# Kernel optimization log

Measured on AMD Instinct MI355X. Metric: run time of the kernel, lower is better.

The kernel has to match this reference:

```python
import jax, jax.numpy as jnp
import numpy as np

IN_FEA = 128
OUT_FEA = 128
ALPHA = 0.2  # LeakyReLU negative slope
NEG_INF = -1.0e12


def setup_inputs() -> dict:
    key = jax.random.key(0)
    k1, k2, k3, k4 = jax.random.split(key, 4)
    b, n = 8, 2048
    inp = jax.random.normal(k1, (b, n, IN_FEA), dtype=jnp.float32)
    adj = jax.random.randint(k2, (b, n, n), 0, 2, dtype=jnp.int32)
    # xavier_uniform with gain=1.414
    def xavier(k, shape, gain=1.414):
        fan_in, fan_out = shape[0], shape[1]
        limit = gain * np.sqrt(6.0 / (fan_in + fan_out))
        return jax.random.uniform(k, shape, jnp.float32, -limit, limit)
    W = xavier(k3, (IN_FEA, OUT_FEA))
    a = xavier(k4, (2 * OUT_FEA, 1))
    return {"inp": inp, "adj": adj, "W": W, "a": a}


def reference(inp, adj, W, a):
    # h: [b, n, d]
    h = jnp.matmul(inp, W)
    # Original builds [b, n*n, 2d] via repeat/view; equivalently split a into
    # a1 (applied to h_j, the 'chunks' half) and a2 (applied to h_i).
    d = h.shape[-1]
    a1 = a[:d, 0]   # [d]
    a2 = a[d:, 0]   # [d]
    f1 = jnp.einsum('bnd,d->bn', h, a1)  # contributes per-column (j)
    f2 = jnp.einsum('bnd,d->bn', h, a2)  # contributes per-row (i)
    e = jax.nn.leaky_relu(f2[:, :, None] + f1[:, None, :], negative_slope=ALPHA)  # [b, n, n]
    logits = jnp.where(adj > 0, e, NEG_INF)
    attention = jax.nn.softmax(logits, axis=-1)
    out_h = jnp.matmul(attention, h)
    out_h = jax.nn.elu(out_h) + h  # concat=True branch
    return out_h
```

## Files before the change

### kernel.cpp

```cpp
#include <hip/hip_runtime.h>
#include <hip/hip_bf16.h>

typedef __bf16 bf16x8 __attribute__((ext_vector_type(8)));
typedef float  f32x4  __attribute__((ext_vector_type(4)));

#define LRELU_ALPHA 0.2f
#define LOG2E 1.44269504088896340736f

__device__ __forceinline__ float fexp2(float x) {
#if __has_builtin(__builtin_amdgcn_exp2f)
    return __builtin_amdgcn_exp2f(x);
#else
    float r; asm("v_exp_f32 %0, %1" : "=v"(r) : "v"(x)); return r;
#endif
}

__device__ __forceinline__ void wg_barrier() {
    asm volatile("s_waitcnt lgkmcnt(0)" ::: "memory");
    __builtin_amdgcn_s_barrier();
    asm volatile("" ::: "memory");
}

__global__ __launch_bounds__(128) void gat_prep(
    const float* __restrict__ inp, const float* __restrict__ W,
    const float* __restrict__ a,
    __bf16* __restrict__ hb, float* __restrict__ f1, float* __restrict__ f2)
{
    const int r0 = blockIdx.x << 3;
    const int d  = threadIdx.x;
    __shared__ float sIn[8][128];
    __shared__ float sRed[8][4];
    #pragma unroll
    for (int r = 0; r < 8; ++r)
        sIn[r][d] = inp[(size_t)(r0 + r) * 128 + d];
    __syncthreads();

    float acc[8] = {0.f,0.f,0.f,0.f,0.f,0.f,0.f,0.f};
    #pragma unroll 4
    for (int k = 0; k < 128; ++k) {
        float wv = W[k * 128 + d];
        #pragma unroll
        for (int r = 0; r < 8; ++r) acc[r] += sIn[r][k] * wv;
    }

    const float a1 = a[d], a2 = a[128 + d];
    const int wv = d >> 6;
    #pragma unroll
    for (int r = 0; r < 8; ++r) {
        hb[(size_t)(r0 + r) * 128 + d] = (__bf16)acc[r];
        float t1 = acc[r] * a1;
        float t2 = acc[r] * a2;
        #pragma unroll
        for (int m = 1; m < 64; m <<= 1) {
            t1 += __shfl_xor(t1, m);
            t2 += __shfl_xor(t2, m);
        }
        if ((d & 63) == 0) { sRed[r][wv] = t1; sRed[r][2 + wv] = t2; }
    }
    __syncthreads();
    if (d < 8) {
        f1[r0 + d] = (sRed[d][0] + sRed[d][1]) * LOG2E;
        f2[r0 + d] = (sRed[d][2] + sRed[d][3]) * LOG2E;
    }
}

__global__ __launch_bounds__(256) void gat_f1max(
    const float* __restrict__ f1, float* __restrict__ f1max)
{
    const int b = blockIdx.x;
    const int t = threadIdx.x;
    float m = -1e30f;
    for (int j = t; j < 2048; j += 256) m = fmaxf(m, f1[b * 2048 + j]);
    #pragma unroll
    for (int k = 1; k < 64; k <<= 1) m = fmaxf(m, __shfl_xor(m, k));
    __shared__ float sm[4];
    if ((t & 63) == 0) sm[t >> 6] = m;
    __syncthreads();
    if (t == 0) f1max[b] = fmaxf(fmaxf(sm[0], sm[1]), fmaxf(sm[2], sm[3]));
}

__global__ __launch_bounds__(256) void gat_pack(
    const __bf16* __restrict__ hb, __bf16* __restrict__ pack)
{
    __shared__ __bf16 tile[64][72];
    const int tid = threadIdx.x;
    const int bidx = blockIdx.x;
    const int b  = bidx >> 6;
    const int tI = bidx & 63;
    const int n0 = (tI >> 1) << 6;
    const int d0 = (tI & 1) << 6;
    #pragma unroll
    for (int pass = 0; pass < 2; ++pass) {
        int row = (tid >> 3) + (pass << 5);
        int c   = (tid & 7) << 3;
        *(bf16x8*)&tile[row][c] =
            *(const bf16x8*)(hb + (size_t)(b * 2048 + n0 + row) * 128 + d0 + c);
    }
    __syncthreads();
    const int lane = tid & 63;
    const int il = lane & 15;
    const int kg = lane >> 4;
    #pragma unroll
    for (int pass = 0; pass < 2; ++pass) {
        const int f  = (tid >> 6) + (pass << 2);
        const int Dl = f >> 1;
        const int jh = f & 1;
        union { __bf16 e[8]; bf16x8 v; } u;
        #pragma unroll
        for (int e = 0; e < 8; ++e)
            u.e[e] = tile[(jh << 5) + (kg << 3) + e][(Dl << 4) + il];
        const size_t off = (((size_t)(b << 5) + (n0 >> 6)) << 13)
                         + ((size_t)((((d0 >> 4) + Dl) << 1) | jh) << 9)
                         + (lane << 3);
        *(bf16x8*)(pack + off) = u.v;
    }
}

__global__ __launch_bounds__(512, 4) void gat_attn13(
    const int* __restrict__ adj, const __bf16* __restrict__ pack,
    const float* __restrict__ f1g, const float* __restrict__ f2g,
    const float* __restrict__ f1maxg,
    float* __restrict__ out, __bf16* __restrict__ pO, float* __restrict__ pD)
{
    const int bid = ((blockIdx.x & 7) << 6) | (blockIdx.x >> 3);
    const int b  = bid >> 6;
    const int rg = (bid >> 2) & 15;
    const int jq = bid & 3;
    const int i0 = rg << 7;
    const int jb = jq << 9;
    const int tid = threadIdx.x;

    __shared__ float us[512];
    __shared__ float vs[512];
    __shared__ alignas(16) __bf16 Bs[2][4096];

    const int w    = tid >> 6;
    const int lane = tid & 63;
    const int il   = lane & 15;
    const int kg   = lane >> 4;

    if (tid < 128) {
        float4 fv = *(const float4*)&f1g[(b << 11) + jb + (tid << 2)];
        float4 uu, vv;
        uu.x = fexp2(fv.x); uu.y = fexp2(fv.y);
        uu.z = fexp2(fv.z); uu.w = fexp2(fv.w);
        vv.x = fexp2(LRELU_ALPHA * fv.x); vv.y = fexp2(LRELU_ALPHA * fv.y);
        vv.z = fexp2(LRELU_ALPHA * fv.z); vv.w = fexp2(LRELU_ALPHA * fv.w);
        *(float4*)&us[tid << 2] = uu;
        *(float4*)&vs[tid << 2] = vv;
    }

    const int row  = i0 + (w << 4) + il;
    const float fm  = f1maxg[b];
    const float f2v = f2g[(b << 11) + row];
    const float zM  = f2v + fm;
    const float M   = fmaxf(zM, LRELU_ALPHA * zM);
    const float ai_ = fexp2(f2v - M);
    const float bi_ = fexp2(__builtin_fmaf(LRELU_ALPHA, f2v, -M));

    const int* ap = adj + (((size_t)(b << 11) + row) << 11) + jb + (kg << 3);

    const __bf16* pkB = pack + (((size_t)(b << 5) + (jq << 3)) << 13)
                      + ((w << 1) << 9) + (lane << 3);

    f32x4 acc[8];
    #pragma unroll
    for (int D = 0; D < 8; ++D) acc[D] = (f32x4){0.f, 0.f, 0.f, 0.f};
    f32x4 accd = {0.f, 0.f, 0.f, 0.f};
    union { __bf16 e[8]; bf16x8 v; } ones;
    #pragma unroll
    for (int x = 0; x < 8; ++x) ones.e[x] = (__bf16)1.0f;
    const bf16x8 onesv = ones.v;

    int4 adjx[2], adjy[2];
    int4 sg = *(const int4*)(pkB);
    adjx[0] = *(const int4*)(ap);
    adjy[0] = *(const int4*)(ap + 4);
    adjx[1] = *(const int4*)(ap + 32);
    adjy[1] = *(const int4*)(ap + 36);
    *(int4*)&Bs[0][(w << 9) + (lane << 3)] = sg;
    sg = *(const int4*)(pkB + 512);

    wg_barrier();

    #pragma unroll
    for (int t = 0; t < 16; ++t) {
        const int cb = t & 1;

        bf16x8 Bf[8];
        #pragma unroll
        for (int D = 0; D < 8; ++D)
            Bf[D] = *(const bf16x8*)&Bs[cb][(D << 9) + (lane << 3)];

        const int4 ax = adjx[t & 1];
        const int4 ay = adjy[t & 1];
        const float4 u0 = *(const float4*)&us[t * 32 + (kg << 3)];
        const float4 u1 = *(const float4*)&us[t * 32 + (kg << 3) + 4];
        const float4 v0 = *(const float4*)&vs[t * 32 + (kg << 3)];
        const float4 v1 = *(const float4*)&vs[t * 32 + (kg << 3) + 4];
        union { __bf16 e[8]; bf16x8 v; } pa;
        pa.e[0] = (ax.x > 0) ? (__bf16)fmaxf(ai_ * u0.x, bi_ * v0.x) : (__bf16)0.f;
        pa.e[1] = (ax.y > 0) ? (__bf16)fmaxf(ai_ * u0.y, bi_ * v0.y) : (__bf16)0.f;
        pa.e[2] = (ax.z > 0) ? (__bf16)fmaxf(ai_ * u0.z, bi_ * v0.z) : (__bf16)0.f;
        pa.e[3] = (ax.w > 0) ? (__bf16)fmaxf(ai_ * u0.w, bi_ * v0.w) : (__bf16)0.f;
        pa.e[4] = (ay.x > 0) ? (__bf16)fmaxf(ai_ * u1.x, bi_ * v1.x) : (__bf16)0.f;
        pa.e[5] = (ay.y > 0) ? (__bf16)fmaxf(ai_ * u1.y, bi_ * v1.y) : (__bf16)0.f;
        pa.e[6] = (ay.z > 0) ? (__bf16)fmaxf(ai_ * u1.z, bi_ * v1.z) : (__bf16)0.f;
        pa.e[7] = (ay.w > 0) ? (__bf16)fmaxf(ai_ * u1.w, bi_ * v1.w) : (__bf16)0.f;

        if (t + 2 < 16) {
            adjx[t & 1] = *(const int4*)(ap + (t + 2) * 32);
            adjy[t & 1] = *(const int4*)(ap + (t + 2) * 32 + 4);
        }

        #pragma unroll
        for (int D = 0; D < 8; ++D)
            acc[D] = __builtin_amdgcn_mfma_f32_16x16x32_bf16(pa.v, Bf[D], acc[D], 0, 0, 0);
        accd = __builtin_amdgcn_mfma_f32_16x16x32_bf16(pa.v, onesv, accd, 0, 0, 0);

        if (t < 15) {
            *(int4*)&Bs[cb ^ 1][(w << 9) + (lane << 3)] = sg;
            if (t < 14)
                sg = *(const int4*)(pkB + (((t + 2) >> 1) << 13) + (((t + 2) & 1) << 9));
            wg_barrier();
        }
    }

    const int rowg = (b << 11) + i0 + (w << 4) + (kg << 2);
    if (jq == 0) {
        #pragma unroll
        for (int r = 0; r < 4; ++r) {
            const size_t base = (((size_t)rowg + r) << 7) + il;
            #pragma unroll
            for (int D = 0; D < 8; ++D)
                out[base + (D << 4)] = acc[D][r];
        }
    } else {
        __bf16* po = pO + ((size_t)(jq - 1) << 21);
        #pragma unroll
        for (int r = 0; r < 4; ++r) {
            const size_t base = (((size_t)rowg + r) << 7) + il;
            #pragma unroll
            for (int D = 0; D < 8; ++D)
                po[base + (D << 4)] = (__bf16)acc[D][r];
        }
    }
    if (il == 0) {
        #pragma unroll
        for (int r = 0; r < 4; ++r)
            pD[(jq << 14) + rowg + r] = accd[r];
    }
}

__global__ __launch_bounds__(256) void gat_combine(
    float* io, const __bf16* __restrict__ pO,
    const float* __restrict__ pD, const __bf16* __restrict__ hb)
{
    const int idx = blockIdx.x * 256 + threadIdx.x;
    const size_t base = (size_t)idx << 3;
    const int rowAll = idx >> 4;
    const float den = pD[rowAll] + pD[16384 + rowAll]
                    + pD[32768 + rowAll] + pD[49152 + rowAll];
    const float rden = 1.0f / den;
    float4 o0a = *(const float4*)(io + base);
    float4 o0b = *(const float4*)(io + base + 4);
    bf16x8 p1 = *(const bf16x8*)(pO + base);
    bf16x8 p2 = *(const bf16x8*)(pO + (1u << 21) + base);
    bf16x8 p3 = *(const bf16x8*)(pO + (2u << 21) + base);
    bf16x8 hv = *(const bf16x8*)(hb + base);
    float res[8];
    #pragma unroll
    for (int e = 0; e < 8; ++e) {
        float o = ((e < 4) ? ((const float*)&o0a)[e] : ((const float*)&o0b)[e - 4])
                + (float)p1[e] + (float)p2[e] + (float)p3[e];
        float v  = o * rden;
        float el = (v > 0.f) ? v : (fexp2(v * LOG2E) - 1.f);
        res[e] = el + (float)hv[e];
    }
    *(float4*)(io + base)     = (float4){res[0], res[1], res[2], res[3]};
    *(float4*)(io + base + 4) = (float4){res[4], res[5], res[6], res[7]};
}

extern "C" void kernel_launch(void* const* d_in, const int* in_sizes, int n_in,
                              void* d_out, int out_size, void* d_ws, size_t ws_size,
                              hipStream_t stream)
{
    const float* inp = (const float*)d_in[0];
    const int*   adj = (const int*)d_in[1];
    const float* W   = (const float*)d_in[2];
    const float* a   = (const float*)d_in[3];
    float* out = (float*)d_out;

    char* ws = (char*)d_ws;
    __bf16* hb    = (__bf16*)ws;
    __bf16* pack  = (__bf16*)(ws + (4 << 20));
    __bf16* pO    = (__bf16*)(ws + (8 << 20));
    float*  pD    = (float*)(ws + (20 << 20));
    float*  f1    = (float*)(ws + (20 << 20) + 262144);
    float*  f2    = (float*)(ws + (20 << 20) + 262144 + 65536);
    float*  f1max = (float*)(ws + (20 << 20) + 262144 + 131072);

    gat_prep<<<2048, 128, 0, stream>>>(inp, W, a, hb, f1, f2);
    gat_f1max<<<8, 256, 0, stream>>>(f1, f1max);
    gat_pack<<<512, 256, 0, stream>>>(hb, pack);
    gat_attn13<<<512, 512, 0, stream>>>(adj, pack, f1, f2, f1max, out, pO, pD);
    gat_combine<<<1024, 256, 0, stream>>>(out, pO, pD, hb);
}
```

Baseline: 62.62 us.

## Deepen prefetch pipeline in GAT attention kernel and interleave LDS reads with MFMA

Rewrites the software pipeline of the attention kernel. Adjacency prefetch goes from two to four tiles ahead and the packed-h prefetch from one to two stages, using two register slots. The initial global loads are issued before the exp2 setup so their latency overlaps it. The shared-memory store for the next buffer now happens at the start of each iteration, B fragments are loaded one at a time just before each MFMA, and the MFMA block is wrapped in s_setprio. This hides global and LDS latency at the cost of more registers, which may pressure occupancy under the 512x4 launch bound.

```diff
diff --git a/kernel.cpp b/kernel.cpp
--- a/kernel.cpp
+++ b/kernel.cpp
@@ -116,7 +116,7 @@
     }
 }
 
-__global__ __launch_bounds__(512, 4) void gat_attn13(
+__global__ __launch_bounds__(512, 4) void gat_attn14(
     const int* __restrict__ adj, const __bf16* __restrict__ pack,
     const float* __restrict__ f1g, const float* __restrict__ f2g,
     const float* __restrict__ f1maxg,
@@ -139,18 +139,33 @@
     const int il   = lane & 15;
     const int kg   = lane >> 4;
 
+    float4 fvl;
+    if (tid < 128) fvl = *(const float4*)&f1g[(b << 11) + jb + (tid << 2)];
+
+    const __bf16* pkB = pack + (((size_t)(b << 5) + (jq << 3)) << 13)
+                      + ((w << 1) << 9) + (lane << 3);
+    bf16x8 b0  = *(const bf16x8*)(pkB);
+    bf16x8 sg1 = *(const bf16x8*)(pkB + 512);
+    bf16x8 sg0 = *(const bf16x8*)(pkB + 8192);
+
+    const int row = i0 + (w << 4) + il;
+    const int* ap = adj + (((size_t)(b << 11) + row) << 11) + jb + (kg << 3);
+    int4 ax[4], ay[4];
+    ax[0] = *(const int4*)(ap);       ay[0] = *(const int4*)(ap + 4);
+    ax[1] = *(const int4*)(ap + 32);  ay[1] = *(const int4*)(ap + 36);
+    ax[2] = *(const int4*)(ap + 64);  ay[2] = *(const int4*)(ap + 68);
+    ax[3] = *(const int4*)(ap + 96);  ay[3] = *(const int4*)(ap + 100);
+
     if (tid < 128) {
-        float4 fv = *(const float4*)&f1g[(b << 11) + jb + (tid << 2)];
         float4 uu, vv;
-        uu.x = fexp2(fv.x); uu.y = fexp2(fv.y);
-        uu.z = fexp2(fv.z); uu.w = fexp2(fv.w);
-        vv.x = fexp2(LRELU_ALPHA * fv.x); vv.y = fexp2(LRELU_ALPHA * fv.y);
-        vv.z = fexp2(LRELU_ALPHA * fv.z); vv.w = fexp2(LRELU_ALPHA * fv.w);
+        uu.x = fexp2(fvl.x); uu.y = fexp2(fvl.y);
+        uu.z = fexp2(fvl.z); uu.w = fexp2(fvl.w);
+        vv.x = fexp2(LRELU_ALPHA * fvl.x); vv.y = fexp2(LRELU_ALPHA * fvl.y);
+        vv.z = fexp2(LRELU_ALPHA * fvl.z); vv.w = fexp2(LRELU_ALPHA * fvl.w);
         *(float4*)&us[tid << 2] = uu;
         *(float4*)&vs[tid << 2] = vv;
     }
 
-    const int row  = i0 + (w << 4) + il;
     const float fm  = f1maxg[b];
     const float f2v = f2g[(b << 11) + row];
     const float zM  = f2v + fm;
@@ -158,11 +173,6 @@
     const float ai_ = fexp2(f2v - M);
     const float bi_ = fexp2(__builtin_fmaf(LRELU_ALPHA, f2v, -M));
 
-    const int* ap = adj + (((size_t)(b << 11) + row) << 11) + jb + (kg << 3);
-
-    const __bf16* pkB = pack + (((size_t)(b << 5) + (jq << 3)) << 13)
-                      + ((w << 1) << 9) + (lane << 3);
-
     f32x4 acc[8];
     #pragma unroll
     for (int D = 0; D < 8; ++D) acc[D] = (f32x4){0.f, 0.f, 0.f, 0.f};
@@ -172,14 +182,7 @@
     for (int x = 0; x < 8; ++x) ones.e[x] = (__bf16)1.0f;
     const bf16x8 onesv = ones.v;
 
-    int4 adjx[2], adjy[2];
-    int4 sg = *(const int4*)(pkB);
-    adjx[0] = *(const int4*)(ap);
-    adjy[0] = *(const int4*)(ap + 4);
-    adjx[1] = *(const int4*)(ap + 32);
-    adjy[1] = *(const int4*)(ap + 36);
-    *(int4*)&Bs[0][(w << 9) + (lane << 3)] = sg;
-    sg = *(const int4*)(pkB + 512);
+    *(bf16x8*)&Bs[0][(w << 9) + (lane << 3)] = b0;
 
     wg_barrier();
 
@@ -187,43 +190,45 @@
     for (int t = 0; t < 16; ++t) {
         const int cb = t & 1;
 
-        bf16x8 Bf[8];
-        #pragma unroll
-        for (int D = 0; D < 8; ++D)
-            Bf[D] = *(const bf16x8*)&Bs[cb][(D << 9) + (lane << 3)];
-
-        const int4 ax = adjx[t & 1];
-        const int4 ay = adjy[t & 1];
+        if (t < 15) {
+            *(bf16x8*)&Bs[cb ^ 1][(w << 9) + (lane << 3)] = (((t + 1) & 1) ? sg1 : sg0);
+        }
+        if (t + 3 <= 15) {
+            bf16x8 nb = *(const bf16x8*)(pkB + (((t + 3) >> 1) << 13) + (((t + 3) & 1) << 9));
+            if (((t + 1) & 1)) sg1 = nb; else sg0 = nb;
+        }
+
+        const int4 axv = ax[t & 3];
+        const int4 ayv = ay[t & 3];
         const float4 u0 = *(const float4*)&us[t * 32 + (kg << 3)];
         const float4 u1 = *(const float4*)&us[t * 32 + (kg << 3) + 4];
         const float4 v0 = *(const float4*)&vs[t * 32 + (kg << 3)];
         const float4 v1 = *(const float4*)&vs[t * 32 + (kg << 3) + 4];
         union { __bf16 e[8]; bf16x8 v; } pa;
-        pa.e[0] = (ax.x > 0) ? (__bf16)fmaxf(ai_ * u0.x, bi_ * v0.x) : (__bf16)0.f;
-        pa.e[1] = (ax.y > 0) ? (__bf16)fmaxf(ai_ * u0.y, bi_ * v0.y) : (__bf16)0.f;
-        pa.e[2] = (ax.z > 0) ? (__bf16)fmaxf(ai_ * u0.z, bi_ * v0.z) : (__bf16)0.f;
-        pa.e[3] = (ax.w > 0) ? (__bf16)fmaxf(ai_ * u0.w, bi_ * v0.w) : (__bf16)0.f;
-        pa.e[4] = (ay.x > 0) ? (__bf16)fmaxf(ai_ * u1.x, bi_ * v1.x) : (__bf16)0.f;
-        pa.e[5] = (ay.y > 0) ? (__bf16)fmaxf(ai_ * u1.y, bi_ * v1.y) : (__bf16)0.f;
-        pa.e[6] = (ay.z > 0) ? (__bf16)fmaxf(ai_ * u1.z, bi_ * v1.z) : (__bf16)0.f;
-        pa.e[7] = (ay.w > 0) ? (__bf16)fmaxf(ai_ * u1.w, bi_ * v1.w) : (__bf16)0.f;
-
-        if (t + 2 < 16) {
-            adjx[t & 1] = *(const int4*)(ap + (t + 2) * 32);
-            adjy[t & 1] = *(const int4*)(ap + (t + 2) * 32 + 4);
-        }
-
-        #pragma unroll
-        for (int D = 0; D < 8; ++D)
-            acc[D] = __builtin_amdgcn_mfma_f32_16x16x32_bf16(pa.v, Bf[D], acc[D], 0, 0, 0);
+        pa.e[0] = (axv.x > 0) ? (__bf16)fmaxf(ai_ * u0.x, bi_ * v0.x) : (__bf16)0.f;
+        pa.e[1] = (axv.y > 0) ? (__bf16)fmaxf(ai_ * u0.y, bi_ * v0.y) : (__bf16)0.f;
+        pa.e[2] = (axv.z > 0) ? (__bf16)fmaxf(ai_ * u0.z, bi_ * v0.z) : (__bf16)0.f;
+        pa.e[3] = (axv.w > 0) ? (__bf16)fmaxf(ai_ * u0.w, bi_ * v0.w) : (__bf16)0.f;
+        pa.e[4] = (ayv.x > 0) ? (__bf16)fmaxf(ai_ * u1.x, bi_ * v1.x) : (__bf16)0.f;
+        pa.e[5] = (ayv.y > 0) ? (__bf16)fmaxf(ai_ * u1.y, bi_ * v1.y) : (__bf16)0.f;
+        pa.e[6] = (ayv.z > 0) ? (__bf16)fmaxf(ai_ * u1.z, bi_ * v1.z) : (__bf16)0.f;
+        pa.e[7] = (ayv.w > 0) ? (__bf16)fmaxf(ai_ * u1.w, bi_ * v1.w) : (__bf16)0.f;
+
+        if (t + 4 < 16) {
+            ax[t & 3] = *(const int4*)(ap + (t + 4) * 32);
+            ay[t & 3] = *(const int4*)(ap + (t + 4) * 32 + 4);
+        }
+
+        __builtin_amdgcn_s_setprio(1);
+        #pragma unroll
+        for (int D = 0; D < 8; ++D) {
+            bf16x8 Bf = *(const bf16x8*)&Bs[cb][(D << 9) + (lane << 3)];
+            acc[D] = __builtin_amdgcn_mfma_f32_16x16x32_bf16(pa.v, Bf, acc[D], 0, 0, 0);
+        }
         accd = __builtin_amdgcn_mfma_f32_16x16x32_bf16(pa.v, onesv, accd, 0, 0, 0);
-
-        if (t < 15) {
-            *(int4*)&Bs[cb ^ 1][(w << 9) + (lane << 3)] = sg;
-            if (t < 14)
-                sg = *(const int4*)(pkB + (((t + 2) >> 1) << 13) + (((t + 2) & 1) << 9));
-            wg_barrier();
-        }
+        __builtin_amdgcn_s_setprio(0);
+
+        if (t < 15) wg_barrier();
     }
 
     const int rowg = (b << 11) + i0 + (w << 4) + (kg << 2);
@@ -303,6 +308,6 @@
     gat_prep<<<2048, 128, 0, stream>>>(inp, W, a, hb, f1, f2);
     gat_f1max<<<8, 256, 0, stream>>>(f1, f1max);
     gat_pack<<<512, 256, 0, stream>>>(hb, pack);
-    gat_attn13<<<512, 512, 0, stream>>>(adj, pack, f1, f2, f1max, out, pO, pD);
+    gat_attn14<<<512, 512, 0, stream>>>(adj, pack, f1, f2, f1max, out, pO, pD);
     gat_combine<<<1024, 256, 0, stream>>>(out, pO, pD, hb);
 }
```

Result: slower. 64.11 us (median of 2 runs) (+2.4%).

## Bit-pack adjacency in a separate kernel and stage B tiles via global_load_lds

Applied to the files above, without the earlier changes.

Adds a pre-pass kernel that reads the int32 adjacency once and packs it into bitmasks, so the attention kernel loads one uint4 mask per lane instead of streaming int32 adjacency inside its main loop. The attention loop now stages the next B tile with a direct global-to-LDS load, uses __syncthreads, loads B fragments lazily inside the MFMA loop, and raises wave priority around the MFMAs. The whole adjacency still has to be read once by the extra kernel, so the change mainly moves that traffic out of the MFMA loop. The cost is one extra launch and a small extra buffer in the workspace.

```diff
diff --git a/kernel.cpp b/kernel.cpp
--- a/kernel.cpp
+++ b/kernel.cpp
@@ -13,12 +13,6 @@
 #else
     float r; asm("v_exp_f32 %0, %1" : "=v"(r) : "v"(x)); return r;
 #endif
-}
-
-__device__ __forceinline__ void wg_barrier() {
-    asm volatile("s_waitcnt lgkmcnt(0)" ::: "memory");
-    __builtin_amdgcn_s_barrier();
-    asm volatile("" ::: "memory");
 }
 
 __global__ __launch_bounds__(128) void gat_prep(
@@ -116,8 +110,67 @@
     }
 }
 
-__global__ __launch_bounds__(512, 4) void gat_attn13(
-    const int* __restrict__ adj, const __bf16* __restrict__ pack,
+__global__ __launch_bounds__(256, 4) void gat_adjpack(
+    const int* __restrict__ adj, uint4* __restrict__ tb)
+{
+    const int tid  = threadIdx.x;
+    const int rloc = tid >> 4;
+    const int jq   = (tid >> 2) & 3;
+    const int kg   = tid & 3;
+    const size_t grow = (size_t)blockIdx.x * 16 + rloc;
+    const int* base = adj + (grow << 11) + (jq << 9) + (kg << 3);
+
+    int4 A[8], B[8];
+    #pragma unroll
+    for (int i = 0; i < 8; ++i)
+        A[i] = *(const int4*)(base + (i >> 1) * 32 + (i & 1) * 4);
+    #pragma unroll
+    for (int i = 0; i < 8; ++i)
+        B[i] = *(const int4*)(base + 128 + (i >> 1) * 32 + (i & 1) * 4);
+
+    unsigned wds[4];
+    #pragma unroll
+    for (int W = 0; W < 4; ++W) {
+        unsigned u = 0;
+        #pragma unroll
+        for (int i = 0; i < 8; ++i) {
+            int4 v = (W & 1) ? B[i] : A[i];
+            const int sh = (i >> 1) * 8 + (i & 1) * 4;
+            u |= ((unsigned)(v.x > 0) << sh)
+               | ((unsigned)(v.y > 0) << (sh + 1))
+               | ((unsigned)(v.z > 0) << (sh + 2))
+               | ((unsigned)(v.w > 0) << (sh + 3));
+        }
+        wds[W] = u;
+        if (W < 2) {
+            #pragma unroll
+            for (int i = 0; i < 8; ++i) {
+                int4 nv = *(const int4*)(base + (W + 2) * 128 + (i >> 1) * 32 + (i & 1) * 4);
+                if (W & 1) B[i] = nv; else A[i] = nv;
+            }
+        }
+    }
+    uint4 o; o.x = wds[0]; o.y = wds[1]; o.z = wds[2]; o.w = wds[3];
+    tb[((grow << 2) + jq) * 4 + kg] = o;
+}
+
+#if __has_builtin(__builtin_amdgcn_global_load_lds)
+#define STAGE(T, BUF)                                                         \
+    __builtin_amdgcn_global_load_lds(                                         \
+        (const __attribute__((address_space(1))) void*)                       \
+            (pkbase + (((T) >> 1) * 16384) + (((T) & 1) * 1024)),             \
+        (__attribute__((address_space(3))) void*)(&Bs[BUF][w << 9]),          \
+        16, 0, 0)
+#else
+#define STAGE(T, BUF) do {                                                    \
+    bf16x8 _tmp = *(const bf16x8*)(pkbase + (((T) >> 1) * 16384)              \
+                                   + (((T) & 1) * 1024));                     \
+    *(bf16x8*)&Bs[BUF][(w << 9) + (lane << 3)] = _tmp;                        \
+} while (0)
+#endif
+
+__global__ __launch_bounds__(512, 4) void gat_attn15(
+    const uint4* __restrict__ tb, const __bf16* __restrict__ pack,
     const float* __restrict__ f1g, const float* __restrict__ f2g,
     const float* __restrict__ f1maxg,
     float* __restrict__ out, __bf16* __restrict__ pO, float* __restrict__ pD)
@@ -130,14 +183,18 @@
     const int jb = jq << 9;
     const int tid = threadIdx.x;
 
-    __shared__ float us[512];
-    __shared__ float vs[512];
+    __shared__ alignas(16) float us[512];
+    __shared__ alignas(16) float vs[512];
     __shared__ alignas(16) __bf16 Bs[2][4096];
 
     const int w    = tid >> 6;
     const int lane = tid & 63;
     const int il   = lane & 15;
     const int kg   = lane >> 4;
+    const int row  = i0 + (w << 4) + il;
+    const size_t grow = (size_t)(b << 11) + row;
+
+    const uint4 mask = tb[((grow << 2) + jq) * 4 + kg];
 
     if (tid < 128) {
         float4 fv = *(const float4*)&f1g[(b << 11) + jb + (tid << 2)];
@@ -150,18 +207,17 @@
         *(float4*)&vs[tid << 2] = vv;
     }
 
-    const int row  = i0 + (w << 4) + il;
     const float fm  = f1maxg[b];
-    const float f2v = f2g[(b << 11) + row];
+    const float f2v = f2g[grow];
     const float zM  = f2v + fm;
     const float M   = fmaxf(zM, LRELU_ALPHA * zM);
     const float ai_ = fexp2(f2v - M);
     const float bi_ = fexp2(__builtin_fmaf(LRELU_ALPHA, f2v, -M));
 
-    const int* ap = adj + (((size_t)(b << 11) + row) << 11) + jb + (kg << 3);
-
-    const __bf16* pkB = pack + (((size_t)(b << 5) + (jq << 3)) << 13)
-                      + ((w << 1) << 9) + (lane << 3);
+    const char* pkbase = (const char*)pack
+        + ((size_t)(b * 32 + jq * 8)) * 16384
+        + (size_t)w * 2048
+        + (size_t)lane * 16;
 
     f32x4 acc[8];
     #pragma unroll
@@ -172,58 +228,42 @@
     for (int x = 0; x < 8; ++x) ones.e[x] = (__bf16)1.0f;
     const bf16x8 onesv = ones.v;
 
-    int4 adjx[2], adjy[2];
-    int4 sg = *(const int4*)(pkB);
-    adjx[0] = *(const int4*)(ap);
-    adjy[0] = *(const int4*)(ap + 4);
-    adjx[1] = *(const int4*)(ap + 32);
-    adjy[1] = *(const int4*)(ap + 36);
-    *(int4*)&Bs[0][(w << 9) + (lane << 3)] = sg;
-    sg = *(const int4*)(pkB + 512);
-
-    wg_barrier();
+    STAGE(0, 0);
+    __syncthreads();
 
     #pragma unroll
     for (int t = 0; t < 16; ++t) {
         const int cb = t & 1;
 
-        bf16x8 Bf[8];
-        #pragma unroll
-        for (int D = 0; D < 8; ++D)
-            Bf[D] = *(const bf16x8*)&Bs[cb][(D << 9) + (lane << 3)];
-
-        const int4 ax = adjx[t & 1];
-        const int4 ay = adjy[t & 1];
+        if (t < 15) STAGE(t + 1, cb ^ 1);
+
+        const unsigned wd = (t >> 2) == 0 ? mask.x : (t >> 2) == 1 ? mask.y
+                          : (t >> 2) == 2 ? mask.z : mask.w;
+        const unsigned byte = (wd >> ((t & 3) << 3)) & 0xffu;
         const float4 u0 = *(const float4*)&us[t * 32 + (kg << 3)];
         const float4 u1 = *(const float4*)&us[t * 32 + (kg << 3) + 4];
         const float4 v0 = *(const float4*)&vs[t * 32 + (kg << 3)];
         const float4 v1 = *(const float4*)&vs[t * 32 + (kg << 3) + 4];
         union { __bf16 e[8]; bf16x8 v; } pa;
-        pa.e[0] = (ax.x > 0) ? (__bf16)fmaxf(ai_ * u0.x, bi_ * v0.x) : (__bf16)0.f;
-        pa.e[1] = (ax.y > 0) ? (__bf16)fmaxf(ai_ * u0.y, bi_ * v0.y) : (__bf16)0.f;
-        pa.e[2] = (ax.z > 0) ? (__bf16)fmaxf(ai_ * u0.z, bi_ * v0.z) : (__bf16)0.f;
-        pa.e[3] = (ax.w > 0) ? (__bf16)fmaxf(ai_ * u0.w, bi_ * v0.w) : (__bf16)0.f;
-        pa.e[4] = (ay.x > 0) ? (__bf16)fmaxf(ai_ * u1.x, bi_ * v1.x) : (__bf16)0.f;
-        pa.e[5] = (ay.y > 0) ? (__bf16)fmaxf(ai_ * u1.y, bi_ * v1.y) : (__bf16)0.f;
-        pa.e[6] = (ay.z > 0) ? (__bf16)fmaxf(ai_ * u1.z, bi_ * v1.z) : (__bf16)0.f;
-        pa.e[7] = (ay.w > 0) ? (__bf16)fmaxf(ai_ * u1.w, bi_ * v1.w) : (__bf16)0.f;
-
-        if (t + 2 < 16) {
-            adjx[t & 1] = *(const int4*)(ap + (t + 2) * 32);
-            adjy[t & 1] = *(const int4*)(ap + (t + 2) * 32 + 4);
-        }
-
-        #pragma unroll
-        for (int D = 0; D < 8; ++D)
-            acc[D] = __builtin_amdgcn_mfma_f32_16x16x32_bf16(pa.v, Bf[D], acc[D], 0, 0, 0);
+        pa.e[0] = (byte &   1u) ? (__bf16)fmaxf(ai_ * u0.x, bi_ * v0.x) : (__bf16)0.f;
+        pa.e[1] = (byte &   2u) ? (__bf16)fmaxf(ai_ * u0.y, bi_ * v0.y) : (__bf16)0.f;
+        pa.e[2] = (byte &   4u) ? (__bf16)fmaxf(ai_ * u0.z, bi_ * v0.z) : (__bf16)0.f;
+        pa.e[3] = (byte &   8u) ? (__bf16)fmaxf(ai_ * u0.w, bi_ * v0.w) : (__bf16)0.f;
+        pa.e[4] = (byte &  16u) ? (__bf16)fmaxf(ai_ * u1.x, bi_ * v1.x) : (__bf16)0.f;
+        pa.e[5] = (byte &  32u) ? (__bf16)fmaxf(ai_ * u1.y, bi_ * v1.y) : (__bf16)0.f;
+        pa.e[6] = (byte &  64u) ? (__bf16)fmaxf(ai_ * u1.z, bi_ * v1.z) : (__bf16)0.f;
+        pa.e[7] = (byte & 128u) ? (__bf16)fmaxf(ai_ * u1.w, bi_ * v1.w) : (__bf16)0.f;
+
+        __builtin_amdgcn_s_setprio(1);
+        #pragma unroll
+        for (int D = 0; D < 8; ++D) {
+            bf16x8 Bf = *(const bf16x8*)&Bs[cb][(D << 9) + (lane << 3)];
+            acc[D] = __builtin_amdgcn_mfma_f32_16x16x32_bf16(pa.v, Bf, acc[D], 0, 0, 0);
+        }
         accd = __builtin_amdgcn_mfma_f32_16x16x32_bf16(pa.v, onesv, accd, 0, 0, 0);
-
-        if (t < 15) {
-            *(int4*)&Bs[cb ^ 1][(w << 9) + (lane << 3)] = sg;
-            if (t < 14)
-                sg = *(const int4*)(pkB + (((t + 2) >> 1) << 13) + (((t + 2) & 1) << 9));
-            wg_barrier();
-        }
+        __builtin_amdgcn_s_setprio(0);
+
+        if (t < 15) __syncthreads();
     }
 
     const int rowg = (b << 11) + i0 + (w << 4) + (kg << 2);
@@ -294,15 +334,17 @@
     char* ws = (char*)d_ws;
     __bf16* hb    = (__bf16*)ws;
     __bf16* pack  = (__bf16*)(ws + (4 << 20));
-    __bf16* pO    = (__bf16*)(ws + (8 << 20));
-    float*  pD    = (float*)(ws + (20 << 20));
-    float*  f1    = (float*)(ws + (20 << 20) + 262144);
-    float*  f2    = (float*)(ws + (20 << 20) + 262144 + 65536);
-    float*  f1max = (float*)(ws + (20 << 20) + 262144 + 131072);
-
+    uint4*  tb    = (uint4*)(ws + (8 << 20));
+    __bf16* pO    = (__bf16*)(ws + (12 << 20));
+    float*  pD    = (float*)(ws + (24 << 20));
+    float*  f1    = (float*)(ws + (24 << 20) + 262144);
+    float*  f2    = (float*)(ws + (24 << 20) + 262144 + 65536);
+    float*  f1max = (float*)(ws + (24 << 20) + 262144 + 131072);
+
+    gat_adjpack<<<1024, 256, 0, stream>>>(adj, tb);
     gat_prep<<<2048, 128, 0, stream>>>(inp, W, a, hb, f1, f2);
     gat_f1max<<<8, 256, 0, stream>>>(f1, f1max);
     gat_pack<<<512, 256, 0, stream>>>(hb, pack);
-    gat_attn13<<<512, 512, 0, stream>>>(adj, pack, f1, f2, f1max, out, pO, pD);
+    gat_attn15<<<512, 512, 0, stream>>>(tb, pack, f1, f2, f1max, out, pO, pD);
     gat_combine<<<1024, 256, 0, stream>>>(out, pO, pD, hb);
 }
```

New measurement: 76.53 us. 1.22x slower.
